# Kernel tuning notes

Hardware: AMD Instinct MI355X
Metric: run time of the kernel (lower is better)

Reference implementation:

```python
import jax, jax.numpy as jnp
import numpy as np

N_NODES = 50000
N_EDGES = 800000
DIMS = [128, 256, 256]
EPS = 1e-5


def setup_inputs() -> dict:
    key = jax.random.key(0)
    ks = jax.random.split(key, 8)
    x = jax.random.normal(ks[0], (N_NODES, DIMS[0]), dtype=jnp.float32)
    edge_index = jax.random.randint(ks[1], (2, N_EDGES), 0, N_NODES, dtype=jnp.int64)
    inp = {"x": x, "edge_index": edge_index}
    for i in range(2):
        din, dout = DIMS[i], DIMS[i + 1]
        # Glorot init for GCN weight; zeros bias; BN gamma=1, beta=0; PReLU a=0.25
        scale = jnp.sqrt(2.0 / (din + dout)).astype(jnp.float32)
        inp[f"W{i}"] = jax.random.normal(ks[2 + i], (din, dout), dtype=jnp.float32) * scale
        inp[f"b{i}"] = jnp.zeros((dout,), dtype=jnp.float32)
        inp[f"gamma{i}"] = jnp.ones((dout,), dtype=jnp.float32)
        inp[f"beta{i}"] = jnp.zeros((dout,), dtype=jnp.float32)
        inp[f"a{i}"] = jnp.full((1,), 0.25, dtype=jnp.float32)
    return inp


def _gcn_bn_prelu(x, src, dst, w_edge, W, b, gamma, beta, a):
    n = x.shape[0]
    h = x @ W  # [N, dout]
    # symmetric GCN normalization with self-loops already appended to src/dst
    deg = jax.ops.segment_sum(w_edge, dst, num_segments=n)  # [N]
    dinv = jnp.where(deg > 0, jax.lax.rsqrt(deg), 0.0)
    norm = dinv[src] * w_edge * dinv[dst]  # [E+N]
    msgs = h[src] * norm[:, None]  # [E+N, dout] gather + scale
    out = jax.ops.segment_sum(msgs, dst, num_segments=n) + b
    # BatchNorm1d (training-mode batch statistics, biased variance)
    mean = jnp.mean(out, axis=0)
    var = jnp.mean(jnp.square(out - mean), axis=0)
    y = (out - mean) * jax.lax.rsqrt(var + EPS) * gamma + beta
    # PReLU with a single shared parameter
    return jnp.where(y > 0, y, a[0] * y)


def reference(x, edge_index, W0, b0, gamma0, beta0, a0, W1, b1, gamma1, beta1, a1):
    n = x.shape[0]
    loops = jnp.arange(n, dtype=edge_index.dtype)
    src = jnp.concatenate([edge_index[0], loops])
    dst = jnp.concatenate([edge_index[1], loops])
    w_edge = jnp.ones(src.shape[0], dtype=x.dtype)
    h = _gcn_bn_prelu(x, src, dst, w_edge, W0, b0, gamma0, beta0, a0)
    h = _gcn_bn_prelu(h, src, dst, w_edge, W1, b1, gamma1, beta1, a1)
    return h
```

## Files before the change

kernel.cpp:

```cpp
#include <hip/hip_runtime.h>

typedef unsigned int u32;
typedef unsigned short u16;
typedef unsigned long long u64;

using f32x4 = __attribute__((ext_vector_type(4))) float;
using bf16x8 = __attribute__((ext_vector_type(8))) short;

#define BN_EPS 1e-5f

__device__ __forceinline__ float bflo(u32 u) {
    union { u32 u; float f; } v; v.u = u << 16; return v.f;
}
__device__ __forceinline__ float bfhi(u32 u) {
    union { u32 u; float f; } v; v.u = u & 0xffff0000u; return v.f;
}
__device__ __forceinline__ u32 f2bf(float f) {
    union { float f; u32 u; } v; v.f = f;
    return (v.u + 0x7fffu + ((v.u >> 16) & 1u)) >> 16;
}

__global__ void detect_k(const void* ei, int* flag, int nnode) {
    const u64* p = (const u64*)ei;
    int lane = threadIdx.x & 63;
    u64 v = p[lane];
    int ok = (v < (u64)nnode);
    int all64 = __all(ok);
    if (threadIdx.x == 0) *flag = all64 ? 1 : 0;
}

__global__ void deg_count_sh_k(const void* ei, const int* __restrict__ flag,
                               int* __restrict__ degi, int E, int n) {
    int grp = blockIdx.x & 7;
    int lo = (int)(((long long)n * grp) >> 3);
    int hi = (int)(((long long)n * (grp + 1)) >> 3);
    int nb = gridDim.x >> 3;
    int bi = blockIdx.x >> 3;
    int is64 = *flag;
    int i = bi * 256 + threadIdx.x;
    int stride = nb * 256;
    if (is64) {
        const long long* p = (const long long*)ei;
        for (; i < E; i += stride) {
            int d = (int)p[(size_t)E + i];
            if (d >= lo && d < hi) atomicAdd(&degi[d], 1);
        }
    } else {
        const int* p = (const int*)ei;
        for (; i < E; i += stride) {
            int d = p[(size_t)E + i];
            if (d >= lo && d < hi) atomicAdd(&degi[d], 1);
        }
    }
}

__global__ void dinv_k(const int* __restrict__ degi, float* __restrict__ dinv, int n) {
    int i = blockIdx.x * blockDim.x + threadIdx.x;
    int stride = gridDim.x * blockDim.x;
    for (; i < n; i += stride) dinv[i] = rsqrtf((float)(degi[i] + 1));
}

__global__ void block_sum_k(const int* __restrict__ counts, int* __restrict__ bsum, int n) {
    __shared__ int red[4];
    int idx = blockIdx.x * 256 + threadIdx.x;
    int v = (idx < n) ? counts[idx] : 0;
#pragma unroll
    for (int m = 32; m >= 1; m >>= 1) v += __shfl_xor(v, m);
    int lane = threadIdx.x & 63, w = threadIdx.x >> 6;
    if (lane == 0) red[w] = v;
    __syncthreads();
    if (threadIdx.x == 0) bsum[blockIdx.x] = red[0] + red[1] + red[2] + red[3];
}

__global__ void scan_bsum_k(int* bsum, int nb) {
    __shared__ int sd[256];
    int t = threadIdx.x;
    int v = (t < nb) ? bsum[t] : 0;
    sd[t] = v; __syncthreads();
    for (int off = 1; off < 256; off <<= 1) {
        int u = (t >= off) ? sd[t - off] : 0;
        __syncthreads();
        sd[t] += u;
        __syncthreads();
    }
    if (t < nb) bsum[t] = sd[t] - v;
}

__global__ void block_scan_k(const int* __restrict__ counts, const int* __restrict__ bsum,
                             int* __restrict__ rp, int n) {
    __shared__ int sd[256];
    int t = threadIdx.x;
    int idx = blockIdx.x * 256 + t;
    int v = (idx < n) ? counts[idx] : 0;
    sd[t] = v; __syncthreads();
    for (int off = 1; off < 256; off <<= 1) {
        int u = (t >= off) ? sd[t - off] : 0;
        __syncthreads();
        sd[t] += u;
        __syncthreads();
    }
    if (idx < n) rp[idx + 1] = bsum[blockIdx.x] + sd[t];
    if (blockIdx.x == 0 && t == 0) rp[0] = 0;
}

__global__ void csr_fill_sh_k(const void* ei, const int* __restrict__ flag,
                              const int* __restrict__ rp, int* __restrict__ fill,
                              u16* __restrict__ csr, int E, int n) {
    int grp = blockIdx.x & 7;
    int lo = (int)(((long long)n * grp) >> 3);
    int hi = (int)(((long long)n * (grp + 1)) >> 3);
    int nb = gridDim.x >> 3;
    int bi = blockIdx.x >> 3;
    int is64 = *flag;
    int i = bi * 256 + threadIdx.x;
    int stride = nb * 256;
    if (is64) {
        const long long* p = (const long long*)ei;
        for (; i < E; i += stride) {
            int d = (int)p[(size_t)E + i];
            if (d >= lo && d < hi) {
                int s = (int)p[i];
                int pos = atomicAdd(&fill[d], 1);
                csr[rp[d] + pos] = (u16)s;
            }
        }
    } else {
        const int* p = (const int*)ei;
        for (; i < E; i += stride) {
            int d = p[(size_t)E + i];
            if (d >= lo && d < hi) {
                int s = p[i];
                int pos = atomicAdd(&fill[d], 1);
                csr[rp[d] + pos] = (u16)s;
            }
        }
    }
}

__global__ void f32_to_bf16_sm_k(const float* __restrict__ in, u16* __restrict__ out,
                                 const float* __restrict__ dinv, int n) {
    int i = blockIdx.x * blockDim.x + threadIdx.x;
    int stride = gridDim.x * blockDim.x;
    int total = n * 32;
    for (; i < total; i += stride) {
        int row = i >> 5;
        int c0 = (i & 31) * 4;
        float dv = dinv[row];
        float4 v = ((const float4*)in)[i];
        u32 lo = f2bf(dv * v.x) | (f2bf(dv * v.y) << 16);
        u32 hi = f2bf(dv * v.z) | (f2bf(dv * v.w) << 16);
        int slice = c0 >> 5, off = c0 & 31;
        *(uint2*)(out + (size_t)slice * n * 32 + (size_t)row * 32 + off) = make_uint2(lo, hi);
    }
}

__global__ void transpose_w_k(const float* __restrict__ W, u16* __restrict__ Wt,
                              int din, int dout) {
    int i = blockIdx.x * blockDim.x + threadIdx.x;
    int total = din * dout;
    if (i < total) {
        int r = i / dout, c = i % dout;
        Wt[(size_t)c * din + r] = (u16)f2bf(W[i]);
    }
}

__device__ __forceinline__ void add8(uint4 r, float* acc) {
    acc[0] += bflo(r.x); acc[1] += bfhi(r.x);
    acc[2] += bflo(r.y); acc[3] += bfhi(r.y);
    acc[4] += bflo(r.z); acc[5] += bfhi(r.z);
    acc[6] += bflo(r.w); acc[7] += bfhi(r.w);
}

template <int NS>
__global__ __launch_bounds__(256) void aggregate_gp_k(
    const u16* __restrict__ H, u16* __restrict__ O,
    const float* __restrict__ dinv, const int* __restrict__ rp,
    const u16* __restrict__ csr, int n)
{
    int b = blockIdx.x;
    int slice = b % NS;
    int lane = threadIdx.x & 63;
    int g = lane >> 2, li = lane & 3;
    int node = (b / NS) * 64 + (threadIdx.x >> 6) * 16 + g;
    if (node >= n) return;
    const u16* Hs = H + (size_t)slice * n * 32;
    float acc[8];
    {
        uint4 r = *(const uint4*)(Hs + (size_t)node * 32 + li * 8);
        acc[0] = bflo(r.x); acc[1] = bfhi(r.x);
        acc[2] = bflo(r.y); acc[3] = bfhi(r.y);
        acc[4] = bflo(r.z); acc[5] = bfhi(r.z);
        acc[6] = bflo(r.w); acc[7] = bfhi(r.w);
    }

    int e0 = rp[node], e1 = rp[node + 1];
    int e = e0;
    for (; e + 4 <= e1; e += 4) {
        u32 s0 = csr[e];
        u32 s1 = csr[e + 1];
        u32 s2 = csr[e + 2];
        u32 s3 = csr[e + 3];
        uint4 r0 = *(const uint4*)(Hs + (size_t)s0 * 32 + li * 8);
        uint4 r1 = *(const uint4*)(Hs + (size_t)s1 * 32 + li * 8);
        uint4 r2 = *(const uint4*)(Hs + (size_t)s2 * 32 + li * 8);
        uint4 r3 = *(const uint4*)(Hs + (size_t)s3 * 32 + li * 8);
        add8(r0, acc);
        add8(r1, acc);
        add8(r2, acc);
        add8(r3, acc);
    }
    for (; e < e1; ++e) {
        uint4 r = *(const uint4*)(Hs + (size_t)csr[e] * 32 + li * 8);
        add8(r, acc);
    }

    float dv = dinv[node];
    uint4 o;
    o.x = f2bf(acc[0] * dv) | (f2bf(acc[1] * dv) << 16);
    o.y = f2bf(acc[2] * dv) | (f2bf(acc[3] * dv) << 16);
    o.z = f2bf(acc[4] * dv) | (f2bf(acc[5] * dv) << 16);
    o.w = f2bf(acc[6] * dv) | (f2bf(acc[7] * dv) << 16);
    *(uint4*)(O + (size_t)slice * n * 32 + (size_t)node * 32 + li * 8) = o;
}

template <int K, int OUTB>
__global__ __launch_bounds__(256) void gemm_bf16(
    const u16* __restrict__ A, const u16* __restrict__ Bt,
    const float* __restrict__ bias, void* __restrict__ outp,
    float* __restrict__ part, int M, int An)
{
    __shared__ __align__(16) u16 lA[4096];
    __shared__ __align__(16) u16 lB[4096];
    __shared__ float red[256];
    const int tid = threadIdx.x;
    const int lane = tid & 63;
    const int wid = tid >> 6;
    const int wm = wid >> 1, wn = wid & 1;
    const int l15 = lane & 15, khi = lane >> 4;
    const int row0 = blockIdx.x * 128;
    const int col0 = blockIdx.y * 128;

    f32x4 acc[4][4];
#pragma unroll
    for (int i = 0; i < 4; ++i)
#pragma unroll
        for (int j = 0; j < 4; ++j)
            acc[i][j] = (f32x4){0.f, 0.f, 0.f, 0.f};

    if (tid < 256) red[tid] = 0.f;

    for (int k0 = 0; k0 < K; k0 += 32) {
        const u16* Asl = A + (size_t)(k0 >> 5) * An * 32;
#pragma unroll
        for (int t = 0; t < 2; ++t) {
            int c = t * 256 + wid * 64 + lane;
            int r = c & 127, kh = c >> 7;
            int ar = row0 + r; if (ar > M - 1) ar = M - 1;
            const u16* ga = Asl + (size_t)ar * 32 + kh * 8;
            u16* la = &lA[(t * 256 + wid * 64) * 8];
            __builtin_amdgcn_global_load_lds(
                (const __attribute__((address_space(1))) void*)ga,
                (__attribute__((address_space(3))) void*)la, 16, 0, 0);
            const u16* gb = Bt + (size_t)(col0 + r) * K + k0 + kh * 8;
            u16* lb = &lB[(t * 256 + wid * 64) * 8];
            __builtin_amdgcn_global_load_lds(
                (const __attribute__((address_space(1))) void*)gb,
                (__attribute__((address_space(3))) void*)lb, 16, 0, 0);
        }
        __syncthreads();
        bf16x8 afr[4], bfr[4];
#pragma unroll
        for (int mi = 0; mi < 4; ++mi)
            afr[mi] = *(const bf16x8*)&lA[khi * 1024 + (wm * 64 + mi * 16 + l15) * 8];
#pragma unroll
        for (int nj = 0; nj < 4; ++nj)
            bfr[nj] = *(const bf16x8*)&lB[khi * 1024 + (wn * 64 + nj * 16 + l15) * 8];
#pragma unroll
        for (int mi = 0; mi < 4; ++mi)
#pragma unroll
            for (int nj = 0; nj < 4; ++nj)
                acc[mi][nj] = __builtin_amdgcn_mfma_f32_16x16x32_bf16(
                    afr[mi], bfr[nj], acc[mi][nj], 0, 0, 0);
        __syncthreads();
    }

#pragma unroll
    for (int mi = 0; mi < 4; ++mi) {
#pragma unroll
        for (int nj = 0; nj < 4; ++nj) {
            int coll = wn * 64 + nj * 16 + l15;
            int colg = col0 + coll;
            float bsv = bias[colg];
            float s = 0.f, q = 0.f;
#pragma unroll
            for (int i = 0; i < 4; ++i) {
                int rowg = row0 + wm * 64 + mi * 16 + khi * 4 + i;
                if (rowg < M) {
                    float v = acc[mi][nj][i] + bsv;
                    if (OUTB) ((u16*)outp)[(size_t)rowg * 256 + colg] = (u16)f2bf(v);
                    else      ((float*)outp)[(size_t)rowg * 256 + colg] = v;
                    s += v; q += v * v;
                }
            }
            s += __shfl_xor(s, 16); s += __shfl_xor(s, 32);
            q += __shfl_xor(q, 16); q += __shfl_xor(q, 32);
            if (lane < 16) {
                atomicAdd(&red[coll * 2], s);
                atomicAdd(&red[coll * 2 + 1], q);
            }
        }
    }
    __syncthreads();
    if (tid < 256)
        part[(size_t)blockIdx.x * 512 + blockIdx.y * 256 + tid] = red[tid];
}

__global__ __launch_bounds__(256) void bn_stats_k(
    const float* __restrict__ part, const float* __restrict__ gamma,
    const float* __restrict__ beta, float* __restrict__ ss, int nbx, int M)
{
    int wave = threadIdx.x >> 6;
    int lane = threadIdx.x & 63;
    int c = blockIdx.x * 4 + wave;
    int base = (c >> 7) * 256 + (c & 127) * 2;
    float s = 0.f, q = 0.f;
    for (int bx = lane; bx < nbx; bx += 64) {
        float2 v = *(const float2*)&part[(size_t)bx * 512 + base];
        s += v.x; q += v.y;
    }
#pragma unroll
    for (int m = 32; m >= 1; m >>= 1) {
        s += __shfl_xor(s, m);
        q += __shfl_xor(q, m);
    }
    if (lane == 0) {
        float mean = s / (float)M;
        float var = fmaxf(q / (float)M - mean * mean, 0.f);
        float sc = gamma[c] * rsqrtf(var + BN_EPS);
        ss[c] = sc;
        ss[256 + c] = beta[c] - mean * sc;
    }
}

__global__ void bn_prelu_sm_k(const u16* __restrict__ in, u16* __restrict__ out,
                              const float* __restrict__ ss, const float* __restrict__ aptr,
                              const float* __restrict__ dinv, int n) {
    float a = aptr[0];
    int i = blockIdx.x * blockDim.x + threadIdx.x;
    int stride = gridDim.x * blockDim.x;
    int total = n * 32;
    for (; i < total; i += stride) {
        int row = i >> 5;
        int c0 = (i & 31) * 8;
        float dv = dinv[row];
        uint4 u = *(const uint4*)(in + (size_t)row * 256 + c0);
        float f0 = bflo(u.x), f1 = bfhi(u.x), f2 = bflo(u.y), f3 = bfhi(u.y);
        float f4 = bflo(u.z), f5 = bfhi(u.z), f6 = bflo(u.w), f7 = bfhi(u.w);
        float r0 = f0 * ss[c0 + 0] + ss[256 + c0 + 0];
        float r1 = f1 * ss[c0 + 1] + ss[256 + c0 + 1];
        float r2 = f2 * ss[c0 + 2] + ss[256 + c0 + 2];
        float r3 = f3 * ss[c0 + 3] + ss[256 + c0 + 3];
        float r4 = f4 * ss[c0 + 4] + ss[256 + c0 + 4];
        float r5 = f5 * ss[c0 + 5] + ss[256 + c0 + 5];
        float r6 = f6 * ss[c0 + 6] + ss[256 + c0 + 6];
        float r7 = f7 * ss[c0 + 7] + ss[256 + c0 + 7];
        r0 = (r0 > 0.f ? r0 : a * r0) * dv;  r1 = (r1 > 0.f ? r1 : a * r1) * dv;
        r2 = (r2 > 0.f ? r2 : a * r2) * dv;  r3 = (r3 > 0.f ? r3 : a * r3) * dv;
        r4 = (r4 > 0.f ? r4 : a * r4) * dv;  r5 = (r5 > 0.f ? r5 : a * r5) * dv;
        r6 = (r6 > 0.f ? r6 : a * r6) * dv;  r7 = (r7 > 0.f ? r7 : a * r7) * dv;
        uint4 o;
        o.x = f2bf(r0) | (f2bf(r1) << 16);
        o.y = f2bf(r2) | (f2bf(r3) << 16);
        o.z = f2bf(r4) | (f2bf(r5) << 16);
        o.w = f2bf(r6) | (f2bf(r7) << 16);
        int slice = c0 >> 5, off = c0 & 31;
        *(uint4*)(out + (size_t)slice * n * 32 + (size_t)row * 32 + off) = o;
    }
}

template <int INB, int OUTB>
__global__ void bn_prelu_k(const void* __restrict__ in, void* __restrict__ outp,
                           const float* __restrict__ ss,
                           const float* __restrict__ aptr, int nquads) {
    float a = aptr[0];
    int i = blockIdx.x * blockDim.x + threadIdx.x;
    int stride = gridDim.x * blockDim.x;
    for (; i < nquads; i += stride) {
        float v0, v1, v2, v3;
        if (INB) {
            uint2 u = ((const uint2*)in)[i];
            v0 = bflo(u.x); v1 = bfhi(u.x); v2 = bflo(u.y); v3 = bfhi(u.y);
        } else {
            float4 v = ((const float4*)in)[i];
            v0 = v.x; v1 = v.y; v2 = v.z; v3 = v.w;
        }
        int c0 = (i * 4) & 255;
        float r0 = v0 * ss[c0 + 0] + ss[256 + c0 + 0];
        float r1 = v1 * ss[c0 + 1] + ss[256 + c0 + 1];
        float r2 = v2 * ss[c0 + 2] + ss[256 + c0 + 2];
        float r3 = v3 * ss[c0 + 3] + ss[256 + c0 + 3];
        r0 = r0 > 0.f ? r0 : a * r0;
        r1 = r1 > 0.f ? r1 : a * r1;
        r2 = r2 > 0.f ? r2 : a * r2;
        r3 = r3 > 0.f ? r3 : a * r3;
        if (OUTB) {
            u32 lo = f2bf(r0) | (f2bf(r1) << 16);
            u32 hi = f2bf(r2) | (f2bf(r3) << 16);
            ((uint2*)outp)[i] = make_uint2(lo, hi);
        } else {
            ((float4*)outp)[i] = make_float4(r0, r1, r2, r3);
        }
    }
}

extern "C" void kernel_launch(void* const* d_in, const int* in_sizes, int n_in,
                              void* d_out, int out_size, void* d_ws, size_t ws_size,
                              hipStream_t stream) {
    const float* x   = (const float*)d_in[0];
    const void*  ei  = d_in[1];
    const float* W0  = (const float*)d_in[2];
    const float* b0  = (const float*)d_in[3];
    const float* g0  = (const float*)d_in[4];
    const float* be0 = (const float*)d_in[5];
    const float* a0  = (const float*)d_in[6];
    const float* W1  = (const float*)d_in[7];
    const float* b1  = (const float*)d_in[8];
    const float* g1  = (const float*)d_in[9];
    const float* be1 = (const float*)d_in[10];
    const float* a1  = (const float*)d_in[11];
    float* out = (float*)d_out;

    const int n = in_sizes[0] / 128;
    const int E = in_sizes[1] / 2;
    const int nbx = (n + 127) / 128;

    char* ws = (char*)d_ws;
    size_t off = 0;
    auto alloc = [&](size_t bytes) {
        size_t r = off; off += (bytes + 255) & ~(size_t)255; return r;
    };
    size_t o_deg  = alloc((size_t)n * 4);
    size_t o_fill = alloc((size_t)n * 4);
    size_t o_rp   = alloc((size_t)(n + 1) * 4);
    size_t o_bsum = alloc(4096);
    size_t o_flag = alloc(256);
    size_t o_dinv = alloc((size_t)n * 4);
    size_t o_csr  = alloc((size_t)E * 2);
    size_t o_part = alloc((size_t)nbx * 512 * 4);
    size_t o_ss   = alloc(2048);
    size_t o_wt0  = alloc(256 * 128 * 2);
    size_t o_wt1  = alloc(256 * 256 * 2);
    size_t o_xh   = alloc((size_t)n * 128 * 2);
    size_t o_agg0 = alloc((size_t)n * 128 * 2);
    size_t o_y0   = alloc((size_t)n * 256 * 2);
    size_t o_agg1 = alloc((size_t)n * 256 * 2);
    size_t o_z1   = o_xh;

    int*   degi  = (int*)(ws + o_deg);
    int*   fill  = (int*)(ws + o_fill);
    int*   rp    = (int*)(ws + o_rp);
    int*   bsum  = (int*)(ws + o_bsum);
    int*   flag  = (int*)(ws + o_flag);
    float* dinv  = (float*)(ws + o_dinv);
    u16*   csr   = (u16*)(ws + o_csr);
    float* part  = (float*)(ws + o_part);
    float* ssbuf = (float*)(ws + o_ss);
    u16*   wt0   = (u16*)(ws + o_wt0);
    u16*   wt1   = (u16*)(ws + o_wt1);
    u16*   xh    = (u16*)(ws + o_xh);
    u16*   agg0  = (u16*)(ws + o_agg0);
    u16*   y0    = (u16*)(ws + o_y0);
    u16*   agg1  = (u16*)(ws + o_agg1);
    u16*   z1    = (u16*)(ws + o_z1);

    hipMemsetAsync(ws + o_deg, 0, (size_t)n * 4, stream);
    hipMemsetAsync(ws + o_fill, 0, (size_t)n * 4, stream);

    const int gN = (n + 255) / 256;
    const int chunks = (n + 63) / 64;

    detect_k<<<1, 64, 0, stream>>>(ei, flag, n);
    deg_count_sh_k<<<1024, 256, 0, stream>>>(ei, flag, degi, E, n);
    dinv_k<<<gN, 256, 0, stream>>>(degi, dinv, n);
    block_sum_k<<<gN, 256, 0, stream>>>(degi, bsum, n);
    scan_bsum_k<<<1, 256, 0, stream>>>(bsum, gN);
    block_scan_k<<<gN, 256, 0, stream>>>(degi, bsum, rp, n);
    csr_fill_sh_k<<<1024, 256, 0, stream>>>(ei, flag, rp, fill, csr, E, n);

    f32_to_bf16_sm_k<<<4096, 256, 0, stream>>>(x, xh, dinv, n);
    transpose_w_k<<<(128 * 256 + 255) / 256, 256, 0, stream>>>(W0, wt0, 128, 256);
    transpose_w_k<<<(256 * 256 + 255) / 256, 256, 0, stream>>>(W1, wt1, 256, 256);

    const dim3 ggrid(nbx, 2);

    aggregate_gp_k<4><<<4 * chunks, 256, 0, stream>>>(xh, agg0, dinv, rp, csr, n);
    gemm_bf16<128, 1><<<ggrid, 256, 0, stream>>>(agg0, wt0, b0, d_out, part, n, n);
    bn_stats_k<<<64, 256, 0, stream>>>(part, g0, be0, ssbuf, nbx, n);
    bn_prelu_sm_k<<<4096, 256, 0, stream>>>((const u16*)d_out, y0, ssbuf, a0, dinv, n);

    aggregate_gp_k<8><<<8 * chunks, 256, 0, stream>>>(y0, agg1, dinv, rp, csr, n);
    gemm_bf16<256, 1><<<ggrid, 256, 0, stream>>>(agg1, wt1, b1, z1, part, n, n);
    bn_stats_k<<<64, 256, 0, stream>>>(part, g1, be1, ssbuf, nbx, n);
    bn_prelu_k<1, 0><<<4096, 256, 0, stream>>>(z1, out, ssbuf, a1, n * 256 / 4);
}
```

Before: 274.2 us.

## Sort nodes by degree for load-balanced aggregation

Builds a degree histogram, scans it, and scatters node ids into a degree-sorted permutation. The aggregation kernels then process nodes in that order, so the 16 node groups in a wavefront see similar edge counts and spend less time idle waiting on the longest one. This adds three small kernels and a memset. It also adds an indirection that breaks the sequential locality of node rows and of the output writes. Degrees here are roughly Poisson around 17, so the imbalance being removed is modest.

```diff
diff --git a/kernel.cpp b/kernel.cpp
--- a/kernel.cpp
+++ b/kernel.cpp
@@ -101,6 +101,26 @@
     }
     if (idx < n) rp[idx + 1] = bsum[blockIdx.x] + sd[t];
     if (blockIdx.x == 0 && t == 0) rp[0] = 0;
+}
+
+__global__ void deg_hist_k(const int* __restrict__ degi, int* __restrict__ hist, int n) {
+    int i = blockIdx.x * blockDim.x + threadIdx.x;
+    int stride = gridDim.x * blockDim.x;
+    for (; i < n; i += stride) {
+        int d = degi[i]; if (d > 255) d = 255;
+        atomicAdd(&hist[d], 1);
+    }
+}
+
+__global__ void perm_scatter_k(const int* __restrict__ degi, int* __restrict__ hist,
+                               int* __restrict__ perm, int n) {
+    int i = blockIdx.x * blockDim.x + threadIdx.x;
+    int stride = gridDim.x * blockDim.x;
+    for (; i < n; i += stride) {
+        int d = degi[i]; if (d > 255) d = 255;
+        int pos = atomicAdd(&hist[d], 1);
+        perm[pos] = i;
+    }
 }
 
 __global__ void csr_fill_sh_k(const void* ei, const int* __restrict__ flag,
@@ -175,14 +195,15 @@
 __global__ __launch_bounds__(256) void aggregate_gp_k(
     const u16* __restrict__ H, u16* __restrict__ O,
     const float* __restrict__ dinv, const int* __restrict__ rp,
-    const u16* __restrict__ csr, int n)
+    const u16* __restrict__ csr, const int* __restrict__ perm, int n)
 {
     int b = blockIdx.x;
     int slice = b % NS;
     int lane = threadIdx.x & 63;
     int g = lane >> 2, li = lane & 3;
-    int node = (b / NS) * 64 + (threadIdx.x >> 6) * 16 + g;
-    if (node >= n) return;
+    int idx = (b / NS) * 64 + (threadIdx.x >> 6) * 16 + g;
+    if (idx >= n) return;
+    int node = perm[idx];
     const u16* Hs = H + (size_t)slice * n * 32;
     float acc[8];
     {
@@ -444,6 +465,8 @@
     size_t o_rp   = alloc((size_t)(n + 1) * 4);
     size_t o_bsum = alloc(4096);
     size_t o_flag = alloc(256);
+    size_t o_hist = alloc(1024);
+    size_t o_perm = alloc((size_t)n * 4);
     size_t o_dinv = alloc((size_t)n * 4);
     size_t o_csr  = alloc((size_t)E * 2);
     size_t o_part = alloc((size_t)nbx * 512 * 4);
@@ -461,6 +484,8 @@
     int*   rp    = (int*)(ws + o_rp);
     int*   bsum  = (int*)(ws + o_bsum);
     int*   flag  = (int*)(ws + o_flag);
+    int*   hist  = (int*)(ws + o_hist);
+    int*   perm  = (int*)(ws + o_perm);
     float* dinv  = (float*)(ws + o_dinv);
     u16*   csr   = (u16*)(ws + o_csr);
     float* part  = (float*)(ws + o_part);
@@ -475,6 +500,7 @@
 
     hipMemsetAsync(ws + o_deg, 0, (size_t)n * 4, stream);
     hipMemsetAsync(ws + o_fill, 0, (size_t)n * 4, stream);
+    hipMemsetAsync(ws + o_hist, 0, 1024, stream);
 
     const int gN = (n + 255) / 256;
     const int chunks = (n + 63) / 64;
@@ -487,18 +513,22 @@
     block_scan_k<<<gN, 256, 0, stream>>>(degi, bsum, rp, n);
     csr_fill_sh_k<<<1024, 256, 0, stream>>>(ei, flag, rp, fill, csr, E, n);
 
+    deg_hist_k<<<gN, 256, 0, stream>>>(degi, hist, n);
+    scan_bsum_k<<<1, 256, 0, stream>>>(hist, 256);
+    perm_scatter_k<<<gN, 256, 0, stream>>>(degi, hist, perm, n);
+
     f32_to_bf16_sm_k<<<4096, 256, 0, stream>>>(x, xh, dinv, n);
     transpose_w_k<<<(128 * 256 + 255) / 256, 256, 0, stream>>>(W0, wt0, 128, 256);
     transpose_w_k<<<(256 * 256 + 255) / 256, 256, 0, stream>>>(W1, wt1, 256, 256);
 
     const dim3 ggrid(nbx, 2);
 
-    aggregate_gp_k<4><<<4 * chunks, 256, 0, stream>>>(xh, agg0, dinv, rp, csr, n);
+    aggregate_gp_k<4><<<4 * chunks, 256, 0, stream>>>(xh, agg0, dinv, rp, csr, perm, n);
     gemm_bf16<128, 1><<<ggrid, 256, 0, stream>>>(agg0, wt0, b0, d_out, part, n, n);
     bn_stats_k<<<64, 256, 0, stream>>>(part, g0, be0, ssbuf, nbx, n);
     bn_prelu_sm_k<<<4096, 256, 0, stream>>>((const u16*)d_out, y0, ssbuf, a0, dinv, n);
 
-    aggregate_gp_k<8><<<8 * chunks, 256, 0, stream>>>(y0, agg1, dinv, rp, csr, n);
+    aggregate_gp_k<8><<<8 * chunks, 256, 0, stream>>>(y0, agg1, dinv, rp, csr, perm, n);
     gemm_bf16<256, 1><<<ggrid, 256, 0, stream>>>(agg1, wt1, b1, z1, part, n, n);
     bn_stats_k<<<64, 256, 0, stream>>>(part, g1, be1, ssbuf, nbx, n);
     bn_prelu_k<1, 0><<<4096, 256, 0, stream>>>(z1, out, ssbuf, a1, n * 256 / 4);
```

Measured after the change: 567.1 us. +106.8%, slower.

## Fuse setup kernels, pad CSR rows to 4, and vectorize index loads

Applied to the files above, without the earlier changes.

Folds the int64-detection kernel into the degree-count and CSR-fill kernels, merges dinv with the block-sum step, and merges the x and weight conversions into one kernel. This cuts the number of launches and collapses the two memsets into one. Each CSR row is padded to a multiple of 4 so the aggregation loop can fetch four neighbour indices with a single ushort4 load, using degi for the row end. Grid sizes of the elementwise kernels are halved. The padding costs a little extra workspace, and every block of the count and fill kernels now re-reads the edge index to detect its width.

```diff
diff --git a/kernel.cpp b/kernel.cpp
--- a/kernel.cpp
+++ b/kernel.cpp
@@ -20,23 +20,19 @@
     return (v.u + 0x7fffu + ((v.u >> 16) & 1u)) >> 16;
 }
 
-__global__ void detect_k(const void* ei, int* flag, int nnode) {
+__device__ __forceinline__ int detect64(const void* ei, int n) {
     const u64* p = (const u64*)ei;
-    int lane = threadIdx.x & 63;
-    u64 v = p[lane];
-    int ok = (v < (u64)nnode);
-    int all64 = __all(ok);
-    if (threadIdx.x == 0) *flag = all64 ? 1 : 0;
-}
-
-__global__ void deg_count_sh_k(const void* ei, const int* __restrict__ flag,
-                               int* __restrict__ degi, int E, int n) {
+    u64 v = p[threadIdx.x & 63];
+    return __all(v < (u64)n) ? 1 : 0;
+}
+
+__global__ void deg_count_sh_k(const void* ei, int* __restrict__ degi, int E, int n) {
+    int is64 = detect64(ei, n);
     int grp = blockIdx.x & 7;
     int lo = (int)(((long long)n * grp) >> 3);
     int hi = (int)(((long long)n * (grp + 1)) >> 3);
     int nb = gridDim.x >> 3;
     int bi = blockIdx.x >> 3;
-    int is64 = *flag;
     int i = bi * 256 + threadIdx.x;
     int stride = nb * 256;
     if (is64) {
@@ -54,16 +50,16 @@
     }
 }
 
-__global__ void dinv_k(const int* __restrict__ degi, float* __restrict__ dinv, int n) {
-    int i = blockIdx.x * blockDim.x + threadIdx.x;
-    int stride = gridDim.x * blockDim.x;
-    for (; i < n; i += stride) dinv[i] = rsqrtf((float)(degi[i] + 1));
-}
-
-__global__ void block_sum_k(const int* __restrict__ counts, int* __restrict__ bsum, int n) {
+__global__ void prep_k(const int* __restrict__ degi, float* __restrict__ dinv,
+                       int* __restrict__ bsum, int n) {
     __shared__ int red[4];
     int idx = blockIdx.x * 256 + threadIdx.x;
-    int v = (idx < n) ? counts[idx] : 0;
+    int v = 0;
+    if (idx < n) {
+        int d = degi[idx];
+        dinv[idx] = rsqrtf((float)(d + 1));
+        v = (d + 3) & ~3;
+    }
 #pragma unroll
     for (int m = 32; m >= 1; m >>= 1) v += __shfl_xor(v, m);
     int lane = threadIdx.x & 63, w = threadIdx.x >> 6;
@@ -91,7 +87,7 @@
     __shared__ int sd[256];
     int t = threadIdx.x;
     int idx = blockIdx.x * 256 + t;
-    int v = (idx < n) ? counts[idx] : 0;
+    int v = (idx < n) ? ((counts[idx] + 3) & ~3) : 0;
     sd[t] = v; __syncthreads();
     for (int off = 1; off < 256; off <<= 1) {
         int u = (t >= off) ? sd[t - off] : 0;
@@ -103,15 +99,15 @@
     if (blockIdx.x == 0 && t == 0) rp[0] = 0;
 }
 
-__global__ void csr_fill_sh_k(const void* ei, const int* __restrict__ flag,
-                              const int* __restrict__ rp, int* __restrict__ fill,
-                              u16* __restrict__ csr, int E, int n) {
+__global__ void csr_fill_sh_k(const void* ei, const int* __restrict__ rp,
+                              int* __restrict__ fill, u16* __restrict__ csr,
+                              int E, int n) {
+    int is64 = detect64(ei, n);
     int grp = blockIdx.x & 7;
     int lo = (int)(((long long)n * grp) >> 3);
     int hi = (int)(((long long)n * (grp + 1)) >> 3);
     int nb = gridDim.x >> 3;
     int bi = blockIdx.x >> 3;
-    int is64 = *flag;
     int i = bi * 256 + threadIdx.x;
     int stride = nb * 256;
     if (is64) {
@@ -137,30 +133,36 @@
     }
 }
 
-__global__ void f32_to_bf16_sm_k(const float* __restrict__ in, u16* __restrict__ out,
-                                 const float* __restrict__ dinv, int n) {
-    int i = blockIdx.x * blockDim.x + threadIdx.x;
-    int stride = gridDim.x * blockDim.x;
-    int total = n * 32;
-    for (; i < total; i += stride) {
-        int row = i >> 5;
-        int c0 = (i & 31) * 4;
-        float dv = dinv[row];
-        float4 v = ((const float4*)in)[i];
-        u32 lo = f2bf(dv * v.x) | (f2bf(dv * v.y) << 16);
-        u32 hi = f2bf(dv * v.z) | (f2bf(dv * v.w) << 16);
-        int slice = c0 >> 5, off = c0 & 31;
-        *(uint2*)(out + (size_t)slice * n * 32 + (size_t)row * 32 + off) = make_uint2(lo, hi);
-    }
-}
-
-__global__ void transpose_w_k(const float* __restrict__ W, u16* __restrict__ Wt,
-                              int din, int dout) {
-    int i = blockIdx.x * blockDim.x + threadIdx.x;
-    int total = din * dout;
-    if (i < total) {
-        int r = i / dout, c = i % dout;
-        Wt[(size_t)c * din + r] = (u16)f2bf(W[i]);
+__global__ void convert_all_k(const float* __restrict__ x, u16* __restrict__ xh,
+                              const float* __restrict__ dinv,
+                              const float* __restrict__ W0, u16* __restrict__ wt0,
+                              const float* __restrict__ W1, u16* __restrict__ wt1,
+                              int n) {
+    int i = blockIdx.x * 256 + threadIdx.x;
+    int stride = gridDim.x * 256;
+    int t0 = n * 32;
+    int t1 = t0 + 128 * 256;
+    int t2 = t1 + 256 * 256;
+    for (; i < t2; i += stride) {
+        if (i < t0) {
+            int row = i >> 5;
+            int c0 = (i & 31) * 4;
+            float dv = dinv[row];
+            float4 v = ((const float4*)x)[i];
+            u32 lo = f2bf(dv * v.x) | (f2bf(dv * v.y) << 16);
+            u32 hi = f2bf(dv * v.z) | (f2bf(dv * v.w) << 16);
+            int slice = c0 >> 5, off = c0 & 31;
+            *(uint2*)(xh + (size_t)slice * n * 32 + (size_t)row * 32 + off) =
+                make_uint2(lo, hi);
+        } else if (i < t1) {
+            int j = i - t0;
+            int r = j >> 8, c = j & 255;
+            wt0[(size_t)c * 128 + r] = (u16)f2bf(W0[j]);
+        } else {
+            int j = i - t1;
+            int r = j >> 8, c = j & 255;
+            wt1[(size_t)c * 256 + r] = (u16)f2bf(W1[j]);
+        }
     }
 }
 
@@ -175,7 +177,7 @@
 __global__ __launch_bounds__(256) void aggregate_gp_k(
     const u16* __restrict__ H, u16* __restrict__ O,
     const float* __restrict__ dinv, const int* __restrict__ rp,
-    const u16* __restrict__ csr, int n)
+    const int* __restrict__ degi, const u16* __restrict__ csr, int n)
 {
     int b = blockIdx.x;
     int slice = b % NS;
@@ -193,17 +195,15 @@
         acc[6] = bflo(r.w); acc[7] = bfhi(r.w);
     }
 
-    int e0 = rp[node], e1 = rp[node + 1];
+    int e0 = rp[node];
+    int e1 = e0 + degi[node];
     int e = e0;
     for (; e + 4 <= e1; e += 4) {
-        u32 s0 = csr[e];
-        u32 s1 = csr[e + 1];
-        u32 s2 = csr[e + 2];
-        u32 s3 = csr[e + 3];
-        uint4 r0 = *(const uint4*)(Hs + (size_t)s0 * 32 + li * 8);
-        uint4 r1 = *(const uint4*)(Hs + (size_t)s1 * 32 + li * 8);
-        uint4 r2 = *(const uint4*)(Hs + (size_t)s2 * 32 + li * 8);
-        uint4 r3 = *(const uint4*)(Hs + (size_t)s3 * 32 + li * 8);
+        ushort4 s4 = *(const ushort4*)&csr[e];
+        uint4 r0 = *(const uint4*)(Hs + (size_t)s4.x * 32 + li * 8);
+        uint4 r1 = *(const uint4*)(Hs + (size_t)s4.y * 32 + li * 8);
+        uint4 r2 = *(const uint4*)(Hs + (size_t)s4.z * 32 + li * 8);
+        uint4 r3 = *(const uint4*)(Hs + (size_t)s4.w * 32 + li * 8);
         add8(r0, acc);
         add8(r1, acc);
         add8(r2, acc);
@@ -443,9 +443,8 @@
     size_t o_fill = alloc((size_t)n * 4);
     size_t o_rp   = alloc((size_t)(n + 1) * 4);
     size_t o_bsum = alloc(4096);
-    size_t o_flag = alloc(256);
     size_t o_dinv = alloc((size_t)n * 4);
-    size_t o_csr  = alloc((size_t)E * 2);
+    size_t o_csr  = alloc(((size_t)E + 4 * n) * 2);
     size_t o_part = alloc((size_t)nbx * 512 * 4);
     size_t o_ss   = alloc(2048);
     size_t o_wt0  = alloc(256 * 128 * 2);
@@ -460,7 +459,6 @@
     int*   fill  = (int*)(ws + o_fill);
     int*   rp    = (int*)(ws + o_rp);
     int*   bsum  = (int*)(ws + o_bsum);
-    int*   flag  = (int*)(ws + o_flag);
     float* dinv  = (float*)(ws + o_dinv);
     u16*   csr   = (u16*)(ws + o_csr);
     float* part  = (float*)(ws + o_part);
@@ -473,33 +471,28 @@
     u16*   agg1  = (u16*)(ws + o_agg1);
     u16*   z1    = (u16*)(ws + o_z1);
 
-    hipMemsetAsync(ws + o_deg, 0, (size_t)n * 4, stream);
-    hipMemsetAsync(ws + o_fill, 0, (size_t)n * 4, stream);
+    hipMemsetAsync(ws + o_deg, 0, (o_fill - o_deg) + (size_t)n * 4, stream);
 
     const int gN = (n + 255) / 256;
     const int chunks = (n + 63) / 64;
 
-    detect_k<<<1, 64, 0, stream>>>(ei, flag, n);
-    deg_count_sh_k<<<1024, 256, 0, stream>>>(ei, flag, degi, E, n);
-    dinv_k<<<gN, 256, 0, stream>>>(degi, dinv, n);
-    block_sum_k<<<gN, 256, 0, stream>>>(degi, bsum, n);
+    deg_count_sh_k<<<1024, 256, 0, stream>>>(ei, degi, E, n);
+    prep_k<<<gN, 256, 0, stream>>>(degi, dinv, bsum, n);
     scan_bsum_k<<<1, 256, 0, stream>>>(bsum, gN);
     block_scan_k<<<gN, 256, 0, stream>>>(degi, bsum, rp, n);
-    csr_fill_sh_k<<<1024, 256, 0, stream>>>(ei, flag, rp, fill, csr, E, n);
-
-    f32_to_bf16_sm_k<<<4096, 256, 0, stream>>>(x, xh, dinv, n);
-    transpose_w_k<<<(128 * 256 + 255) / 256, 256, 0, stream>>>(W0, wt0, 128, 256);
-    transpose_w_k<<<(256 * 256 + 255) / 256, 256, 0, stream>>>(W1, wt1, 256, 256);
+    csr_fill_sh_k<<<1024, 256, 0, stream>>>(ei, rp, fill, csr, E, n);
+
+    convert_all_k<<<2048, 256, 0, stream>>>(x, xh, dinv, W0, wt0, W1, wt1, n);
 
     const dim3 ggrid(nbx, 2);
 
-    aggregate_gp_k<4><<<4 * chunks, 256, 0, stream>>>(xh, agg0, dinv, rp, csr, n);
+    aggregate_gp_k<4><<<4 * chunks, 256, 0, stream>>>(xh, agg0, dinv, rp, degi, csr, n);
     gemm_bf16<128, 1><<<ggrid, 256, 0, stream>>>(agg0, wt0, b0, d_out, part, n, n);
     bn_stats_k<<<64, 256, 0, stream>>>(part, g0, be0, ssbuf, nbx, n);
-    bn_prelu_sm_k<<<4096, 256, 0, stream>>>((const u16*)d_out, y0, ssbuf, a0, dinv, n);
-
-    aggregate_gp_k<8><<<8 * chunks, 256, 0, stream>>>(y0, agg1, dinv, rp, csr, n);
+    bn_prelu_sm_k<<<2048, 256, 0, stream>>>((const u16*)d_out, y0, ssbuf, a0, dinv, n);
+
+    aggregate_gp_k<8><<<8 * chunks, 256, 0, stream>>>(y0, agg1, dinv, rp, degi, csr, n);
     gemm_bf16<256, 1><<<ggrid, 256, 0, stream>>>(agg1, wt1, b1, z1, part, n, n);
     bn_stats_k<<<64, 256, 0, stream>>>(part, g1, be1, ssbuf, nbx, n);
-    bn_prelu_k<1, 0><<<4096, 256, 0, stream>>>(z1, out, ssbuf, a1, n * 256 / 4);
-}
+    bn_prelu_k<1, 0><<<2048, 256, 0, stream>>>(z1, out, ssbuf, a1, n * 256 / 4);
+}
```

Result: faster. 268.2 us (-2.2%).
